# Performance work log

Measured on AMD Instinct MI355X. Metric: run time of the kernel, lower is better.

The kernel has to match this reference:

```python
import jax, jax.numpy as jnp
import numpy as np

N_NODES = 100000
N_EDGES = 1600000
IN_DIM = 48
HID = 16
N_CLASSES = 8


def _sage_conv(x, src, dst, W_l, W_r, b, n_nodes):
    # PyG SAGEConv (aggr='mean', root_weight=True):
    #   out_i = W_l @ mean_{j in N(i)} x_j + b + W_r @ x_i
    msg = x[src]                                              # [E, F]
    agg = jax.ops.segment_sum(msg, dst, num_segments=n_nodes)  # [N, F]
    deg = jax.ops.segment_sum(jnp.ones((src.shape[0],), x.dtype), dst,
                              num_segments=n_nodes)            # [N]
    agg = agg / jnp.maximum(deg, 1.0)[:, None]
    return agg @ W_l.T + b + x @ W_r.T


def setup_inputs() -> dict:
    key = jax.random.key(0)
    ks = jax.random.split(key, 10)
    def lin(k, out_d, in_d):
        s = 1.0 / np.sqrt(in_d)
        return jax.random.uniform(k, (out_d, in_d), jnp.float32, -s, s)
    x = jax.random.normal(ks[0], (N_NODES, IN_DIM), jnp.float32)
    edge_index = jax.random.randint(ks[1], (2, N_EDGES), 0, N_NODES, jnp.int64)
    return {
        "x": x,
        "edge_index": edge_index,
        "W1_l": lin(ks[2], HID, IN_DIM), "W1_r": lin(ks[3], HID, IN_DIM),
        "b1": jnp.zeros((HID,), jnp.float32),
        "W2_l": lin(ks[4], HID, HID), "W2_r": lin(ks[5], HID, HID),
        "b2": jnp.zeros((HID,), jnp.float32),
        "W3_l": lin(ks[6], N_CLASSES, HID), "W3_r": lin(ks[7], N_CLASSES, HID),
        "b3": jnp.zeros((N_CLASSES,), jnp.float32),
    }


def reference(x, edge_index, W1_l, W1_r, b1, W2_l, W2_r, b2, W3_l, W3_r, b3):
    src, dst = edge_index[0], edge_index[1]
    n = x.shape[0]
    # dropout is identity in deterministic/eval reference
    h = jax.nn.elu(_sage_conv(x, src, dst, W1_l, W1_r, b1, n))
    h = jax.nn.elu(_sage_conv(h, src, dst, W2_l, W2_r, b2, n))
    h = jax.nn.elu(_sage_conv(h, src, dst, W3_l, W3_r, b3, n))
    return jax.nn.log_softmax(h, axis=-1)
```

## Files before the change

### kernel.cpp

```cpp
#include <hip/hip_runtime.h>
#include <hip/hip_bf16.h>
#include <math.h>

#define N_IN   48
#define N_HID  16
#define N_CLS  8
#define CAP    48
#define NB_SHIFT 9
#define TILE   4096
#define WSTR   52

__device__ __forceinline__ float bf2f(unsigned short u) {
    union { unsigned int i; float f; } c;
    c.i = ((unsigned int)u) << 16;
    return c.f;
}
__device__ __forceinline__ unsigned short f2bf(float f) {
    unsigned int u = __float_as_uint(f);
    unsigned int r = u + 0x7FFFu + ((u >> 16) & 1u);
    return (unsigned short)(r >> 16);
}

__global__ __launch_bounds__(256) void proj48_kernel(
        const float* __restrict__ X,
        const float* __restrict__ Wl,
        const float* __restrict__ Wr,
        const float* __restrict__ b,
        unsigned short* __restrict__ P,
        float* __restrict__ S,
        int N) {
    __shared__ float sWl[N_HID * WSTR];
    __shared__ float sWr[N_HID * WSTR];
    __shared__ float sb[N_HID];
    int t = threadIdx.x;
    for (int idx = t; idx < N_HID * N_IN; idx += 256) {
        int r = idx / N_IN, k = idx - r * N_IN;
        sWl[r * WSTR + k] = Wl[idx];
        sWr[r * WSTR + k] = Wr[idx];
    }
    if (t < N_HID) sb[t] = b[t];
    __syncthreads();

    int node = blockIdx.x * 64 + (t >> 2);
    int q = t & 3;
    if (node >= N) return;

    const float4* xrow = reinterpret_cast<const float4*>(X + (size_t)node * N_IN);
    float accL[4], accR[4];
#pragma unroll
    for (int oo = 0; oo < 4; oo++) { accL[oo] = 0.0f; accR[oo] = sb[4 * q + oo]; }

#pragma unroll
    for (int c = 0; c < N_IN / 4; c++) {
        float4 xv = xrow[c];
#pragma unroll
        for (int oo = 0; oo < 4; oo++) {
            int row = 4 * q + oo;
            float4 wl = *reinterpret_cast<const float4*>(&sWl[row * WSTR + 4 * c]);
            float4 wr = *reinterpret_cast<const float4*>(&sWr[row * WSTR + 4 * c]);
            accL[oo] = fmaf(xv.x, wl.x, accL[oo]); accR[oo] = fmaf(xv.x, wr.x, accR[oo]);
            accL[oo] = fmaf(xv.y, wl.y, accL[oo]); accR[oo] = fmaf(xv.y, wr.y, accR[oo]);
            accL[oo] = fmaf(xv.z, wl.z, accL[oo]); accR[oo] = fmaf(xv.z, wr.z, accR[oo]);
            accL[oo] = fmaf(xv.w, wl.w, accL[oo]); accR[oo] = fmaf(xv.w, wr.w, accR[oo]);
        }
    }

    int gid = node * 4 + q;
    reinterpret_cast<ushort4*>(P)[gid] =
        make_ushort4(f2bf(accL[0]), f2bf(accL[1]), f2bf(accL[2]), f2bf(accL[3]));
    reinterpret_cast<float4*>(S)[gid] =
        make_float4(accR[0], accR[1], accR[2], accR[3]);
}

__global__ __launch_bounds__(256) void hist0_kernel(
        const int* __restrict__ dst, int* __restrict__ bucketCnt,
        int E, int nbuck) {
    __shared__ int lh[256];
    lh[threadIdx.x] = 0;
    __syncthreads();
    for (int e = blockIdx.x * blockDim.x + threadIdx.x; e < E;
         e += gridDim.x * blockDim.x)
        atomicAdd(&lh[dst[e] >> NB_SHIFT], 1);
    __syncthreads();
    int t = threadIdx.x;
    if (t < nbuck && lh[t]) atomicAdd(&bucketCnt[t], lh[t]);
}

__global__ __launch_bounds__(256) void scan_kernel(
        const int* __restrict__ bucketCnt, int* __restrict__ bucketBase,
        int* __restrict__ cursor, int nbuck, int E) {
    __shared__ int s[256];
    int t = threadIdx.x;
    int v = (t < nbuck) ? bucketCnt[t] : 0;
    s[t] = v;
    __syncthreads();
#pragma unroll
    for (int d = 1; d < 256; d <<= 1) {
        int a = (t >= d) ? s[t - d] : 0;
        __syncthreads();
        s[t] += a;
        __syncthreads();
    }
    if (t < nbuck) {
        int base = s[t] - v;
        bucketBase[t] = base;
        cursor[t] = base;
    }
    if (t == 0) bucketBase[nbuck] = E;
}

__global__ __launch_bounds__(256) void scatter_tiles_kernel(
        const int* __restrict__ src, const int* __restrict__ dst,
        int* __restrict__ cursor, int* __restrict__ ebuf, int E) {
    __shared__ int lh[256];
    __shared__ int gbase[256];
    __shared__ int rank[256];
    int t = threadIdx.x;
    lh[t] = 0;
    rank[t] = 0;
    __syncthreads();
    int base = blockIdx.x * TILE;
#pragma unroll
    for (int k = 0; k < TILE / 256; k++) {
        int e = base + t + k * 256;
        if (e < E) atomicAdd(&lh[dst[e] >> NB_SHIFT], 1);
    }
    __syncthreads();
    if (lh[t]) gbase[t] = atomicAdd(&cursor[t], lh[t]);
    __syncthreads();
#pragma unroll
    for (int k = 0; k < TILE / 256; k++) {
        int e = base + t + k * 256;
        if (e < E) {
            int d = dst[e];
            int b = d >> NB_SHIFT;
            int r = atomicAdd(&rank[b], 1);
            ebuf[gbase[b] + r] = ((d & 511) << 17) | src[e];
        }
    }
}

__global__ __launch_bounds__(256) void fine_fill_kernel(
        const int* __restrict__ bucketBase, const int* __restrict__ ebuf,
        int* __restrict__ cnt, int* __restrict__ adj, int N) {
    __shared__ int lc[512];
    int b = blockIdx.x;
    int nodeBeg = b << NB_SHIFT;
    for (int i = threadIdx.x; i < 512; i += 256) lc[i] = 0;
    __syncthreads();
    int beg = bucketBase[b], end = bucketBase[b + 1];
    for (int e = beg + threadIdx.x; e < end; e += 256) {
        int v = ebuf[e];
        int ld = ((unsigned int)v) >> 17;
        int s  = v & 0x1FFFF;
        int p = atomicAdd(&lc[ld], 1);
        if (p < CAP) adj[(size_t)(nodeBeg + ld) * CAP + p] = s;
    }
    __syncthreads();
    for (int i = threadIdx.x; nodeBeg + i < N && i < 512; i += 256)
        cnt[nodeBeg + i] = lc[i];
}

__global__ __launch_bounds__(256) void gather_proj16_kernel(
        const int* __restrict__ cnt, const int* __restrict__ adj,
        const unsigned short* __restrict__ Pin, const float* __restrict__ Sin,
        const float* __restrict__ Wl, const float* __restrict__ Wr,
        const float* __restrict__ bias,
        unsigned short* __restrict__ Pout, float* __restrict__ Sout, int N) {
    int gid = blockIdx.x * blockDim.x + threadIdx.x;
    if (gid >= N * 4) return;
    int i = gid >> 2;
    int q = gid & 3;
    int deg = cnt[i];
    if (deg > CAP) deg = CAP;
    const int* lst = adj + (size_t)i * CAP;
    float4 acc = make_float4(0.f, 0.f, 0.f, 0.f);
    const ushort4* P4 = reinterpret_cast<const ushort4*>(Pin);
    int e = 0;
    for (; e + 4 <= deg; e += 4) {
        int4 js = *reinterpret_cast<const int4*>(lst + e);
        ushort4 t0 = P4[(size_t)js.x * 4 + q];
        ushort4 t1 = P4[(size_t)js.y * 4 + q];
        ushort4 t2 = P4[(size_t)js.z * 4 + q];
        ushort4 t3 = P4[(size_t)js.w * 4 + q];
        acc.x += bf2f(t0.x) + bf2f(t1.x) + bf2f(t2.x) + bf2f(t3.x);
        acc.y += bf2f(t0.y) + bf2f(t1.y) + bf2f(t2.y) + bf2f(t3.y);
        acc.z += bf2f(t0.z) + bf2f(t1.z) + bf2f(t2.z) + bf2f(t3.z);
        acc.w += bf2f(t0.w) + bf2f(t1.w) + bf2f(t2.w) + bf2f(t3.w);
    }
    for (; e < deg; e++) {
        ushort4 t = P4[(size_t)lst[e] * 4 + q];
        acc.x += bf2f(t.x); acc.y += bf2f(t.y);
        acc.z += bf2f(t.z); acc.w += bf2f(t.w);
    }
    float inv = 1.0f / (float)max(deg, 1);
    float4 sv = reinterpret_cast<const float4*>(Sin)[gid];
    float4 h;
    h.x = acc.x * inv + sv.x; h.y = acc.y * inv + sv.y;
    h.z = acc.z * inv + sv.z; h.w = acc.w * inv + sv.w;
    h.x = h.x > 0.f ? h.x : expm1f(h.x);
    h.y = h.y > 0.f ? h.y : expm1f(h.y);
    h.z = h.z > 0.f ? h.z : expm1f(h.z);
    h.w = h.w > 0.f ? h.w : expm1f(h.w);

    int lane = threadIdx.x & 63;
    int lb = lane & ~3;
    float hv[16];
#pragma unroll
    for (int a = 0; a < 4; a++) {
        hv[4 * a + 0] = __shfl(h.x, lb + a, 64);
        hv[4 * a + 1] = __shfl(h.y, lb + a, 64);
        hv[4 * a + 2] = __shfl(h.z, lb + a, 64);
        hv[4 * a + 3] = __shfl(h.w, lb + a, 64);
    }

    const float4* Wl4 = reinterpret_cast<const float4*>(Wl);
    const float4* Wr4 = reinterpret_cast<const float4*>(Wr);
    float pl[4], sr[4];
#pragma unroll
    for (int oo = 0; oo < 4; oo++) {
        int o = 4 * q + oo;
        float aL = 0.0f, aR = bias[o];
#pragma unroll
        for (int c = 0; c < 4; c++) {
            float4 wl = Wl4[o * 4 + c];
            float4 wr = Wr4[o * 4 + c];
            aL = fmaf(hv[4 * c + 0], wl.x, aL); aR = fmaf(hv[4 * c + 0], wr.x, aR);
            aL = fmaf(hv[4 * c + 1], wl.y, aL); aR = fmaf(hv[4 * c + 1], wr.y, aR);
            aL = fmaf(hv[4 * c + 2], wl.z, aL); aR = fmaf(hv[4 * c + 2], wr.z, aR);
            aL = fmaf(hv[4 * c + 3], wl.w, aL); aR = fmaf(hv[4 * c + 3], wr.w, aR);
        }
        pl[oo] = aL; sr[oo] = aR;
    }
    reinterpret_cast<ushort4*>(Pout)[gid] =
        make_ushort4(f2bf(pl[0]), f2bf(pl[1]), f2bf(pl[2]), f2bf(pl[3]));
    reinterpret_cast<float4*>(Sout)[gid] = make_float4(sr[0], sr[1], sr[2], sr[3]);
}

__global__ __launch_bounds__(256) void gather_proj8_kernel(
        const int* __restrict__ cnt, const int* __restrict__ adj,
        const unsigned short* __restrict__ Pin, const float* __restrict__ Sin,
        const float* __restrict__ Wl, const float* __restrict__ Wr,
        const float* __restrict__ bias,
        unsigned short* __restrict__ Pout, float* __restrict__ Sout, int N) {
    int gid = blockIdx.x * blockDim.x + threadIdx.x;
    if (gid >= N * 4) return;
    int i = gid >> 2;
    int q = gid & 3;
    int deg = cnt[i];
    if (deg > CAP) deg = CAP;
    const int* lst = adj + (size_t)i * CAP;
    float4 acc = make_float4(0.f, 0.f, 0.f, 0.f);
    const ushort4* P4 = reinterpret_cast<const ushort4*>(Pin);
    int e = 0;
    for (; e + 4 <= deg; e += 4) {
        int4 js = *reinterpret_cast<const int4*>(lst + e);
        ushort4 t0 = P4[(size_t)js.x * 4 + q];
        ushort4 t1 = P4[(size_t)js.y * 4 + q];
        ushort4 t2 = P4[(size_t)js.z * 4 + q];
        ushort4 t3 = P4[(size_t)js.w * 4 + q];
        acc.x += bf2f(t0.x) + bf2f(t1.x) + bf2f(t2.x) + bf2f(t3.x);
        acc.y += bf2f(t0.y) + bf2f(t1.y) + bf2f(t2.y) + bf2f(t3.y);
        acc.z += bf2f(t0.z) + bf2f(t1.z) + bf2f(t2.z) + bf2f(t3.z);
        acc.w += bf2f(t0.w) + bf2f(t1.w) + bf2f(t2.w) + bf2f(t3.w);
    }
    for (; e < deg; e++) {
        ushort4 t = P4[(size_t)lst[e] * 4 + q];
        acc.x += bf2f(t.x); acc.y += bf2f(t.y);
        acc.z += bf2f(t.z); acc.w += bf2f(t.w);
    }
    float inv = 1.0f / (float)max(deg, 1);
    float4 sv = reinterpret_cast<const float4*>(Sin)[gid];
    float4 h;
    h.x = acc.x * inv + sv.x; h.y = acc.y * inv + sv.y;
    h.z = acc.z * inv + sv.z; h.w = acc.w * inv + sv.w;
    h.x = h.x > 0.f ? h.x : expm1f(h.x);
    h.y = h.y > 0.f ? h.y : expm1f(h.y);
    h.z = h.z > 0.f ? h.z : expm1f(h.z);
    h.w = h.w > 0.f ? h.w : expm1f(h.w);

    int lane = threadIdx.x & 63;
    int lb = lane & ~3;
    float hv[16];
#pragma unroll
    for (int a = 0; a < 4; a++) {
        hv[4 * a + 0] = __shfl(h.x, lb + a, 64);
        hv[4 * a + 1] = __shfl(h.y, lb + a, 64);
        hv[4 * a + 2] = __shfl(h.z, lb + a, 64);
        hv[4 * a + 3] = __shfl(h.w, lb + a, 64);
    }

    const float4* Wl4 = reinterpret_cast<const float4*>(Wl);
    const float4* Wr4 = reinterpret_cast<const float4*>(Wr);
    float pl[2], sr[2];
#pragma unroll
    for (int oo = 0; oo < 2; oo++) {
        int o = 2 * q + oo;
        float aL = 0.0f, aR = bias[o];
#pragma unroll
        for (int c = 0; c < 4; c++) {
            float4 wl = Wl4[o * 4 + c];
            float4 wr = Wr4[o * 4 + c];
            aL = fmaf(hv[4 * c + 0], wl.x, aL); aR = fmaf(hv[4 * c + 0], wr.x, aR);
            aL = fmaf(hv[4 * c + 1], wl.y, aL); aR = fmaf(hv[4 * c + 1], wr.y, aR);
            aL = fmaf(hv[4 * c + 2], wl.z, aL); aR = fmaf(hv[4 * c + 2], wr.z, aR);
            aL = fmaf(hv[4 * c + 3], wl.w, aL); aR = fmaf(hv[4 * c + 3], wr.w, aR);
        }
        pl[oo] = aL; sr[oo] = aR;
    }
    unsigned int packed = ((unsigned int)f2bf(pl[1]) << 16) | f2bf(pl[0]);
    reinterpret_cast<unsigned int*>(Pout)[gid] = packed;
    reinterpret_cast<float2*>(Sout)[gid] = make_float2(sr[0], sr[1]);
}

__global__ __launch_bounds__(256) void gather8_kernel(
        const int* __restrict__ cnt, const int* __restrict__ adj,
        const unsigned short* __restrict__ P, const float* __restrict__ S,
        float* __restrict__ out, int N) {
    int gid = blockIdx.x * blockDim.x + threadIdx.x;
    if (gid >= N * 2) return;
    int i = gid >> 1;
    int q = gid & 1;
    int deg = cnt[i];
    if (deg > CAP) deg = CAP;
    const int* lst = adj + (size_t)i * CAP;
    float4 acc = make_float4(0.f, 0.f, 0.f, 0.f);
    const ushort4* P4 = reinterpret_cast<const ushort4*>(P);
    int e = 0;
    for (; e + 4 <= deg; e += 4) {
        int4 js = *reinterpret_cast<const int4*>(lst + e);
        ushort4 t0 = P4[(size_t)js.x * 2 + q];
        ushort4 t1 = P4[(size_t)js.y * 2 + q];
        ushort4 t2 = P4[(size_t)js.z * 2 + q];
        ushort4 t3 = P4[(size_t)js.w * 2 + q];
        acc.x += bf2f(t0.x) + bf2f(t1.x) + bf2f(t2.x) + bf2f(t3.x);
        acc.y += bf2f(t0.y) + bf2f(t1.y) + bf2f(t2.y) + bf2f(t3.y);
        acc.z += bf2f(t0.z) + bf2f(t1.z) + bf2f(t2.z) + bf2f(t3.z);
        acc.w += bf2f(t0.w) + bf2f(t1.w) + bf2f(t2.w) + bf2f(t3.w);
    }
    for (; e < deg; e++) {
        ushort4 t = P4[(size_t)lst[e] * 2 + q];
        acc.x += bf2f(t.x); acc.y += bf2f(t.y);
        acc.z += bf2f(t.z); acc.w += bf2f(t.w);
    }
    float inv = 1.0f / (float)max(deg, 1);
    float4 sv = reinterpret_cast<const float4*>(S)[gid];
    float4 v;
    v.x = acc.x * inv + sv.x; v.y = acc.y * inv + sv.y;
    v.z = acc.z * inv + sv.z; v.w = acc.w * inv + sv.w;
    v.x = v.x > 0.f ? v.x : expm1f(v.x);
    v.y = v.y > 0.f ? v.y : expm1f(v.y);
    v.z = v.z > 0.f ? v.z : expm1f(v.z);
    v.w = v.w > 0.f ? v.w : expm1f(v.w);
    float m = fmaxf(fmaxf(v.x, v.y), fmaxf(v.z, v.w));
    m = fmaxf(m, __shfl_xor(m, 1));
    float sum = expf(v.x - m) + expf(v.y - m) + expf(v.z - m) + expf(v.w - m);
    sum += __shfl_xor(sum, 1);
    float lse = m + logf(sum);
    reinterpret_cast<float4*>(out)[gid] =
        make_float4(v.x - lse, v.y - lse, v.z - lse, v.w - lse);
}

extern "C" void kernel_launch(void* const* d_in, const int* in_sizes, int n_in,
                              void* d_out, int out_size, void* d_ws, size_t ws_size,
                              hipStream_t stream) {
    const float* x   = (const float*)d_in[0];
    const int*   ei  = (const int*)d_in[1];
    const float* W1l = (const float*)d_in[2];
    const float* W1r = (const float*)d_in[3];
    const float* b1  = (const float*)d_in[4];
    const float* W2l = (const float*)d_in[5];
    const float* W2r = (const float*)d_in[6];
    const float* b2  = (const float*)d_in[7];
    const float* W3l = (const float*)d_in[8];
    const float* W3r = (const float*)d_in[9];
    const float* b3  = (const float*)d_in[10];
    float* out = (float*)d_out;

    const int N = in_sizes[0] / N_IN;
    const int E = in_sizes[1] / 2;
    const int* src = ei;
    const int* dst = ei + E;
    const int nbuck = (N + 511) >> NB_SHIFT;

    int* bucketCnt  = (int*)d_ws;
    int* bucketBase = bucketCnt + 512;
    int* cursor     = bucketBase + 512;
    int* cnt        = cursor + 512;
    int  Npad       = (N + 3) & ~3;
    int* adj        = cnt + Npad;
    unsigned short* P1 = (unsigned short*)(adj + (size_t)N * CAP);
    unsigned short* P2 = P1 + (size_t)N * N_HID;
    float* S1 = (float*)(P2 + (size_t)N * N_HID);
    float* S3 = S1 + (size_t)N * N_HID;
    int* ebuf = (int*)P1;
    unsigned short* P3 = P1;

    hipMemsetAsync(bucketCnt, 0, 512 * sizeof(int), stream);

    const int B = 256;
    int n4Grid   = (N * 4 + B - 1) / B;
    int n2Grid   = (N * 2 + B - 1) / B;
    int p1Grid   = (N + 63) / 64;
    int tileGrid = (E + TILE - 1) / TILE;

    hist0_kernel<<<512, B, 0, stream>>>(dst, bucketCnt, E, nbuck);
    scan_kernel<<<1, 256, 0, stream>>>(bucketCnt, bucketBase, cursor, nbuck, E);
    scatter_tiles_kernel<<<tileGrid, B, 0, stream>>>(src, dst, cursor, ebuf, E);
    fine_fill_kernel<<<nbuck, B, 0, stream>>>(bucketBase, ebuf, cnt, adj, N);

    proj48_kernel<<<p1Grid, B, 0, stream>>>(x, W1l, W1r, b1, P1, S1, N);

    gather_proj16_kernel<<<n4Grid, B, 0, stream>>>(cnt, adj, P1, S1,
                                                   W2l, W2r, b2, P2, S1, N);

    gather_proj8_kernel<<<n4Grid, B, 0, stream>>>(cnt, adj, P2, S1,
                                                  W3l, W3r, b3, P3, S3, N);

    gather8_kernel<<<n2Grid, B, 0, stream>>>(cnt, adj, P3, S3, out, N);
}
```

Before: 258.0 us.

## Aggregate neighbors per destination bucket with LDS atomics instead of a per-node adjacency list

Drops the histogram, scan and fine-fill kernels and builds no per-node adjacency list. Edges are scattered into fixed-capacity slots per 512-node destination bucket. Each of the three layers then runs one 512-thread block per bucket that gathers source features and accumulates sums and degrees with shared-memory float atomics, then applies the projection or log-softmax. The root-term S buffers are also stored as bf16 instead of fp32, cutting memory traffic at some cost in precision. Risks: only about 196 blocks, which may underfill the GPU; shared-atomic contention; and silent edge loss if a bucket receives more than 9216 edges.

```diff
diff --git a/kernel.cpp b/kernel.cpp
--- a/kernel.cpp
+++ b/kernel.cpp
@@ -5,10 +5,13 @@
 #define N_IN   48
 #define N_HID  16
 #define N_CLS  8
-#define CAP    48
 #define NB_SHIFT 9
+#define BNODES 512
 #define TILE   4096
+#define CAPB   9216
 #define WSTR   52
+#define ASTR   17
+#define ASTR8  9
 
 __device__ __forceinline__ float bf2f(unsigned short u) {
     union { unsigned int i; float f; } c;
@@ -27,7 +30,7 @@
         const float* __restrict__ Wr,
         const float* __restrict__ b,
         unsigned short* __restrict__ P,
-        float* __restrict__ S,
+        unsigned short* __restrict__ S,
         int N) {
     __shared__ float sWl[N_HID * WSTR];
     __shared__ float sWr[N_HID * WSTR];
@@ -68,45 +71,8 @@
     int gid = node * 4 + q;
     reinterpret_cast<ushort4*>(P)[gid] =
         make_ushort4(f2bf(accL[0]), f2bf(accL[1]), f2bf(accL[2]), f2bf(accL[3]));
-    reinterpret_cast<float4*>(S)[gid] =
-        make_float4(accR[0], accR[1], accR[2], accR[3]);
-}
-
-__global__ __launch_bounds__(256) void hist0_kernel(
-        const int* __restrict__ dst, int* __restrict__ bucketCnt,
-        int E, int nbuck) {
-    __shared__ int lh[256];
-    lh[threadIdx.x] = 0;
-    __syncthreads();
-    for (int e = blockIdx.x * blockDim.x + threadIdx.x; e < E;
-         e += gridDim.x * blockDim.x)
-        atomicAdd(&lh[dst[e] >> NB_SHIFT], 1);
-    __syncthreads();
-    int t = threadIdx.x;
-    if (t < nbuck && lh[t]) atomicAdd(&bucketCnt[t], lh[t]);
-}
-
-__global__ __launch_bounds__(256) void scan_kernel(
-        const int* __restrict__ bucketCnt, int* __restrict__ bucketBase,
-        int* __restrict__ cursor, int nbuck, int E) {
-    __shared__ int s[256];
-    int t = threadIdx.x;
-    int v = (t < nbuck) ? bucketCnt[t] : 0;
-    s[t] = v;
-    __syncthreads();
-#pragma unroll
-    for (int d = 1; d < 256; d <<= 1) {
-        int a = (t >= d) ? s[t - d] : 0;
-        __syncthreads();
-        s[t] += a;
-        __syncthreads();
-    }
-    if (t < nbuck) {
-        int base = s[t] - v;
-        bucketBase[t] = base;
-        cursor[t] = base;
-    }
-    if (t == 0) bucketBase[nbuck] = E;
+    reinterpret_cast<ushort4*>(S)[gid] =
+        make_ushort4(f2bf(accR[0]), f2bf(accR[1]), f2bf(accR[2]), f2bf(accR[3]));
 }
 
 __global__ __launch_bounds__(256) void scatter_tiles_kernel(
@@ -120,10 +86,16 @@
     rank[t] = 0;
     __syncthreads();
     int base = blockIdx.x * TILE;
+    int dcache[TILE / 256];
 #pragma unroll
     for (int k = 0; k < TILE / 256; k++) {
         int e = base + t + k * 256;
-        if (e < E) atomicAdd(&lh[dst[e] >> NB_SHIFT], 1);
+        dcache[k] = -1;
+        if (e < E) {
+            int d = dst[e];
+            dcache[k] = d;
+            atomicAdd(&lh[d >> NB_SHIFT], 1);
+        }
     }
     __syncthreads();
     if (lh[t]) gbase[t] = atomicAdd(&cursor[t], lh[t]);
@@ -132,233 +104,275 @@
     for (int k = 0; k < TILE / 256; k++) {
         int e = base + t + k * 256;
         if (e < E) {
-            int d = dst[e];
+            int d = dcache[k];
             int b = d >> NB_SHIFT;
-            int r = atomicAdd(&rank[b], 1);
-            ebuf[gbase[b] + r] = ((d & 511) << 17) | src[e];
-        }
-    }
-}
-
-__global__ __launch_bounds__(256) void fine_fill_kernel(
-        const int* __restrict__ bucketBase, const int* __restrict__ ebuf,
-        int* __restrict__ cnt, int* __restrict__ adj, int N) {
-    __shared__ int lc[512];
-    int b = blockIdx.x;
-    int nodeBeg = b << NB_SHIFT;
-    for (int i = threadIdx.x; i < 512; i += 256) lc[i] = 0;
-    __syncthreads();
-    int beg = bucketBase[b], end = bucketBase[b + 1];
-    for (int e = beg + threadIdx.x; e < end; e += 256) {
-        int v = ebuf[e];
-        int ld = ((unsigned int)v) >> 17;
-        int s  = v & 0x1FFFF;
-        int p = atomicAdd(&lc[ld], 1);
-        if (p < CAP) adj[(size_t)(nodeBeg + ld) * CAP + p] = s;
-    }
-    __syncthreads();
-    for (int i = threadIdx.x; nodeBeg + i < N && i < 512; i += 256)
-        cnt[nodeBeg + i] = lc[i];
-}
-
-__global__ __launch_bounds__(256) void gather_proj16_kernel(
-        const int* __restrict__ cnt, const int* __restrict__ adj,
-        const unsigned short* __restrict__ Pin, const float* __restrict__ Sin,
+            int r = gbase[b] + atomicAdd(&rank[b], 1);
+            if (r < CAPB)
+                ebuf[b * CAPB + r] = ((d & 511) << 17) | src[e];
+        }
+    }
+}
+
+__global__ __launch_bounds__(512) void bucket_gp16_kernel(
+        const int* __restrict__ cursor, const int* __restrict__ ebuf,
+        const unsigned short* __restrict__ Pin, const unsigned short* __restrict__ Sin,
         const float* __restrict__ Wl, const float* __restrict__ Wr,
         const float* __restrict__ bias,
-        unsigned short* __restrict__ Pout, float* __restrict__ Sout, int N) {
-    int gid = blockIdx.x * blockDim.x + threadIdx.x;
-    if (gid >= N * 4) return;
-    int i = gid >> 2;
-    int q = gid & 3;
-    int deg = cnt[i];
-    if (deg > CAP) deg = CAP;
-    const int* lst = adj + (size_t)i * CAP;
-    float4 acc = make_float4(0.f, 0.f, 0.f, 0.f);
+        unsigned short* __restrict__ Pout, unsigned short* __restrict__ Sout, int N) {
+    __shared__ float agg[BNODES * ASTR];
+    __shared__ int   cnt[BNODES];
+    int b = blockIdx.x;
+    int t = threadIdx.x;
+    int nodeBeg = b << NB_SHIFT;
+    for (int i = t; i < BNODES * ASTR; i += 512) agg[i] = 0.0f;
+    if (t < BNODES) cnt[t] = 0;
+    __syncthreads();
+
+    int nb = cursor[b];
+    if (nb > CAPB) nb = CAPB;
+    int beg = b * CAPB, end = beg + nb;
+    int quad = t >> 2, q = t & 3;
     const ushort4* P4 = reinterpret_cast<const ushort4*>(Pin);
-    int e = 0;
-    for (; e + 4 <= deg; e += 4) {
-        int4 js = *reinterpret_cast<const int4*>(lst + e);
-        ushort4 t0 = P4[(size_t)js.x * 4 + q];
-        ushort4 t1 = P4[(size_t)js.y * 4 + q];
-        ushort4 t2 = P4[(size_t)js.z * 4 + q];
-        ushort4 t3 = P4[(size_t)js.w * 4 + q];
-        acc.x += bf2f(t0.x) + bf2f(t1.x) + bf2f(t2.x) + bf2f(t3.x);
-        acc.y += bf2f(t0.y) + bf2f(t1.y) + bf2f(t2.y) + bf2f(t3.y);
-        acc.z += bf2f(t0.z) + bf2f(t1.z) + bf2f(t2.z) + bf2f(t3.z);
-        acc.w += bf2f(t0.w) + bf2f(t1.w) + bf2f(t2.w) + bf2f(t3.w);
-    }
-    for (; e < deg; e++) {
-        ushort4 t = P4[(size_t)lst[e] * 4 + q];
-        acc.x += bf2f(t.x); acc.y += bf2f(t.y);
-        acc.z += bf2f(t.z); acc.w += bf2f(t.w);
-    }
-    float inv = 1.0f / (float)max(deg, 1);
-    float4 sv = reinterpret_cast<const float4*>(Sin)[gid];
-    float4 h;
-    h.x = acc.x * inv + sv.x; h.y = acc.y * inv + sv.y;
-    h.z = acc.z * inv + sv.z; h.w = acc.w * inv + sv.w;
-    h.x = h.x > 0.f ? h.x : expm1f(h.x);
-    h.y = h.y > 0.f ? h.y : expm1f(h.y);
-    h.z = h.z > 0.f ? h.z : expm1f(h.z);
-    h.w = h.w > 0.f ? h.w : expm1f(h.w);
-
-    int lane = threadIdx.x & 63;
-    int lb = lane & ~3;
-    float hv[16];
-#pragma unroll
-    for (int a = 0; a < 4; a++) {
-        hv[4 * a + 0] = __shfl(h.x, lb + a, 64);
-        hv[4 * a + 1] = __shfl(h.y, lb + a, 64);
-        hv[4 * a + 2] = __shfl(h.z, lb + a, 64);
-        hv[4 * a + 3] = __shfl(h.w, lb + a, 64);
-    }
+    int e = beg + quad;
+    for (; e + 128 < end; e += 256) {
+        int v0 = ebuf[e], v1 = ebuf[e + 128];
+        int ld0 = ((unsigned int)v0) >> 17, s0 = v0 & 0x1FFFF;
+        int ld1 = ((unsigned int)v1) >> 17, s1 = v1 & 0x1FFFF;
+        ushort4 p0 = P4[(size_t)s0 * 4 + q];
+        ushort4 p1 = P4[(size_t)s1 * 4 + q];
+        float* a0 = &agg[ld0 * ASTR + 4 * q];
+        float* a1 = &agg[ld1 * ASTR + 4 * q];
+        atomicAdd(a0 + 0, bf2f(p0.x)); atomicAdd(a0 + 1, bf2f(p0.y));
+        atomicAdd(a0 + 2, bf2f(p0.z)); atomicAdd(a0 + 3, bf2f(p0.w));
+        atomicAdd(a1 + 0, bf2f(p1.x)); atomicAdd(a1 + 1, bf2f(p1.y));
+        atomicAdd(a1 + 2, bf2f(p1.z)); atomicAdd(a1 + 3, bf2f(p1.w));
+        if (q == 0) { atomicAdd(&cnt[ld0], 1); atomicAdd(&cnt[ld1], 1); }
+    }
+    for (; e < end; e += 128) {
+        int v = ebuf[e];
+        int ld = ((unsigned int)v) >> 17, s = v & 0x1FFFF;
+        ushort4 p = P4[(size_t)s * 4 + q];
+        float* a = &agg[ld * ASTR + 4 * q];
+        atomicAdd(a + 0, bf2f(p.x)); atomicAdd(a + 1, bf2f(p.y));
+        atomicAdd(a + 2, bf2f(p.z)); atomicAdd(a + 3, bf2f(p.w));
+        if (q == 0) atomicAdd(&cnt[ld], 1);
+    }
+    __syncthreads();
 
     const float4* Wl4 = reinterpret_cast<const float4*>(Wl);
     const float4* Wr4 = reinterpret_cast<const float4*>(Wr);
-    float pl[4], sr[4];
-#pragma unroll
-    for (int oo = 0; oo < 4; oo++) {
-        int o = 4 * q + oo;
-        float aL = 0.0f, aR = bias[o];
-#pragma unroll
-        for (int c = 0; c < 4; c++) {
-            float4 wl = Wl4[o * 4 + c];
-            float4 wr = Wr4[o * 4 + c];
-            aL = fmaf(hv[4 * c + 0], wl.x, aL); aR = fmaf(hv[4 * c + 0], wr.x, aR);
-            aL = fmaf(hv[4 * c + 1], wl.y, aL); aR = fmaf(hv[4 * c + 1], wr.y, aR);
-            aL = fmaf(hv[4 * c + 2], wl.z, aL); aR = fmaf(hv[4 * c + 2], wr.z, aR);
-            aL = fmaf(hv[4 * c + 3], wl.w, aL); aR = fmaf(hv[4 * c + 3], wr.w, aR);
-        }
-        pl[oo] = aL; sr[oo] = aR;
-    }
-    reinterpret_cast<ushort4*>(Pout)[gid] =
-        make_ushort4(f2bf(pl[0]), f2bf(pl[1]), f2bf(pl[2]), f2bf(pl[3]));
-    reinterpret_cast<float4*>(Sout)[gid] = make_float4(sr[0], sr[1], sr[2], sr[3]);
-}
-
-__global__ __launch_bounds__(256) void gather_proj8_kernel(
-        const int* __restrict__ cnt, const int* __restrict__ adj,
-        const unsigned short* __restrict__ Pin, const float* __restrict__ Sin,
+#pragma unroll
+    for (int p = 0; p < 4; p++) {
+        int ln = p * 128 + (t >> 2);
+        int i = nodeBeg + ln;
+        if (i >= N) continue;
+        int gid = i * 4 + q;
+        int deg = cnt[ln];
+        float inv = 1.0f / (float)max(deg, 1);
+        ushort4 svu = reinterpret_cast<const ushort4*>(Sin)[gid];
+        float4 h;
+        h.x = agg[ln * ASTR + 4 * q + 0] * inv + bf2f(svu.x);
+        h.y = agg[ln * ASTR + 4 * q + 1] * inv + bf2f(svu.y);
+        h.z = agg[ln * ASTR + 4 * q + 2] * inv + bf2f(svu.z);
+        h.w = agg[ln * ASTR + 4 * q + 3] * inv + bf2f(svu.w);
+        h.x = h.x > 0.f ? h.x : expm1f(h.x);
+        h.y = h.y > 0.f ? h.y : expm1f(h.y);
+        h.z = h.z > 0.f ? h.z : expm1f(h.z);
+        h.w = h.w > 0.f ? h.w : expm1f(h.w);
+
+        int lane = t & 63;
+        int lb = lane & ~3;
+        float hv[16];
+#pragma unroll
+        for (int a = 0; a < 4; a++) {
+            hv[4 * a + 0] = __shfl(h.x, lb + a, 64);
+            hv[4 * a + 1] = __shfl(h.y, lb + a, 64);
+            hv[4 * a + 2] = __shfl(h.z, lb + a, 64);
+            hv[4 * a + 3] = __shfl(h.w, lb + a, 64);
+        }
+        float pl[4], sr[4];
+#pragma unroll
+        for (int oo = 0; oo < 4; oo++) {
+            int o = 4 * q + oo;
+            float aL = 0.0f, aR = bias[o];
+#pragma unroll
+            for (int c = 0; c < 4; c++) {
+                float4 wl = Wl4[o * 4 + c];
+                float4 wr = Wr4[o * 4 + c];
+                aL = fmaf(hv[4 * c + 0], wl.x, aL); aR = fmaf(hv[4 * c + 0], wr.x, aR);
+                aL = fmaf(hv[4 * c + 1], wl.y, aL); aR = fmaf(hv[4 * c + 1], wr.y, aR);
+                aL = fmaf(hv[4 * c + 2], wl.z, aL); aR = fmaf(hv[4 * c + 2], wr.z, aR);
+                aL = fmaf(hv[4 * c + 3], wl.w, aL); aR = fmaf(hv[4 * c + 3], wr.w, aR);
+            }
+            pl[oo] = aL; sr[oo] = aR;
+        }
+        reinterpret_cast<ushort4*>(Pout)[gid] =
+            make_ushort4(f2bf(pl[0]), f2bf(pl[1]), f2bf(pl[2]), f2bf(pl[3]));
+        reinterpret_cast<ushort4*>(Sout)[gid] =
+            make_ushort4(f2bf(sr[0]), f2bf(sr[1]), f2bf(sr[2]), f2bf(sr[3]));
+    }
+}
+
+__global__ __launch_bounds__(512) void bucket_gp8_kernel(
+        const int* __restrict__ cursor, const int* __restrict__ ebuf,
+        const unsigned short* __restrict__ Pin, const unsigned short* __restrict__ Sin,
         const float* __restrict__ Wl, const float* __restrict__ Wr,
         const float* __restrict__ bias,
-        unsigned short* __restrict__ Pout, float* __restrict__ Sout, int N) {
-    int gid = blockIdx.x * blockDim.x + threadIdx.x;
-    if (gid >= N * 4) return;
-    int i = gid >> 2;
-    int q = gid & 3;
-    int deg = cnt[i];
-    if (deg > CAP) deg = CAP;
-    const int* lst = adj + (size_t)i * CAP;
-    float4 acc = make_float4(0.f, 0.f, 0.f, 0.f);
+        unsigned int* __restrict__ Pout, unsigned int* __restrict__ Sout, int N) {
+    __shared__ float agg[BNODES * ASTR];
+    __shared__ int   cnt[BNODES];
+    int b = blockIdx.x;
+    int t = threadIdx.x;
+    int nodeBeg = b << NB_SHIFT;
+    for (int i = t; i < BNODES * ASTR; i += 512) agg[i] = 0.0f;
+    if (t < BNODES) cnt[t] = 0;
+    __syncthreads();
+
+    int nb = cursor[b];
+    if (nb > CAPB) nb = CAPB;
+    int beg = b * CAPB, end = beg + nb;
+    int quad = t >> 2, q = t & 3;
     const ushort4* P4 = reinterpret_cast<const ushort4*>(Pin);
-    int e = 0;
-    for (; e + 4 <= deg; e += 4) {
-        int4 js = *reinterpret_cast<const int4*>(lst + e);
-        ushort4 t0 = P4[(size_t)js.x * 4 + q];
-        ushort4 t1 = P4[(size_t)js.y * 4 + q];
-        ushort4 t2 = P4[(size_t)js.z * 4 + q];
-        ushort4 t3 = P4[(size_t)js.w * 4 + q];
-        acc.x += bf2f(t0.x) + bf2f(t1.x) + bf2f(t2.x) + bf2f(t3.x);
-        acc.y += bf2f(t0.y) + bf2f(t1.y) + bf2f(t2.y) + bf2f(t3.y);
-        acc.z += bf2f(t0.z) + bf2f(t1.z) + bf2f(t2.z) + bf2f(t3.z);
-        acc.w += bf2f(t0.w) + bf2f(t1.w) + bf2f(t2.w) + bf2f(t3.w);
-    }
-    for (; e < deg; e++) {
-        ushort4 t = P4[(size_t)lst[e] * 4 + q];
-        acc.x += bf2f(t.x); acc.y += bf2f(t.y);
-        acc.z += bf2f(t.z); acc.w += bf2f(t.w);
-    }
-    float inv = 1.0f / (float)max(deg, 1);
-    float4 sv = reinterpret_cast<const float4*>(Sin)[gid];
-    float4 h;
-    h.x = acc.x * inv + sv.x; h.y = acc.y * inv + sv.y;
-    h.z = acc.z * inv + sv.z; h.w = acc.w * inv + sv.w;
-    h.x = h.x > 0.f ? h.x : expm1f(h.x);
-    h.y = h.y > 0.f ? h.y : expm1f(h.y);
-    h.z = h.z > 0.f ? h.z : expm1f(h.z);
-    h.w = h.w > 0.f ? h.w : expm1f(h.w);
-
-    int lane = threadIdx.x & 63;
-    int lb = lane & ~3;
-    float hv[16];
-#pragma unroll
-    for (int a = 0; a < 4; a++) {
-        hv[4 * a + 0] = __shfl(h.x, lb + a, 64);
-        hv[4 * a + 1] = __shfl(h.y, lb + a, 64);
-        hv[4 * a + 2] = __shfl(h.z, lb + a, 64);
-        hv[4 * a + 3] = __shfl(h.w, lb + a, 64);
-    }
+    int e = beg + quad;
+    for (; e + 128 < end; e += 256) {
+        int v0 = ebuf[e], v1 = ebuf[e + 128];
+        int ld0 = ((unsigned int)v0) >> 17, s0 = v0 & 0x1FFFF;
+        int ld1 = ((unsigned int)v1) >> 17, s1 = v1 & 0x1FFFF;
+        ushort4 p0 = P4[(size_t)s0 * 4 + q];
+        ushort4 p1 = P4[(size_t)s1 * 4 + q];
+        float* a0 = &agg[ld0 * ASTR + 4 * q];
+        float* a1 = &agg[ld1 * ASTR + 4 * q];
+        atomicAdd(a0 + 0, bf2f(p0.x)); atomicAdd(a0 + 1, bf2f(p0.y));
+        atomicAdd(a0 + 2, bf2f(p0.z)); atomicAdd(a0 + 3, bf2f(p0.w));
+        atomicAdd(a1 + 0, bf2f(p1.x)); atomicAdd(a1 + 1, bf2f(p1.y));
+        atomicAdd(a1 + 2, bf2f(p1.z)); atomicAdd(a1 + 3, bf2f(p1.w));
+        if (q == 0) { atomicAdd(&cnt[ld0], 1); atomicAdd(&cnt[ld1], 1); }
+    }
+    for (; e < end; e += 128) {
+        int v = ebuf[e];
+        int ld = ((unsigned int)v) >> 17, s = v & 0x1FFFF;
+        ushort4 p = P4[(size_t)s * 4 + q];
+        float* a = &agg[ld * ASTR + 4 * q];
+        atomicAdd(a + 0, bf2f(p.x)); atomicAdd(a + 1, bf2f(p.y));
+        atomicAdd(a + 2, bf2f(p.z)); atomicAdd(a + 3, bf2f(p.w));
+        if (q == 0) atomicAdd(&cnt[ld], 1);
+    }
+    __syncthreads();
 
     const float4* Wl4 = reinterpret_cast<const float4*>(Wl);
     const float4* Wr4 = reinterpret_cast<const float4*>(Wr);
-    float pl[2], sr[2];
-#pragma unroll
-    for (int oo = 0; oo < 2; oo++) {
-        int o = 2 * q + oo;
-        float aL = 0.0f, aR = bias[o];
-#pragma unroll
-        for (int c = 0; c < 4; c++) {
-            float4 wl = Wl4[o * 4 + c];
-            float4 wr = Wr4[o * 4 + c];
-            aL = fmaf(hv[4 * c + 0], wl.x, aL); aR = fmaf(hv[4 * c + 0], wr.x, aR);
-            aL = fmaf(hv[4 * c + 1], wl.y, aL); aR = fmaf(hv[4 * c + 1], wr.y, aR);
-            aL = fmaf(hv[4 * c + 2], wl.z, aL); aR = fmaf(hv[4 * c + 2], wr.z, aR);
-            aL = fmaf(hv[4 * c + 3], wl.w, aL); aR = fmaf(hv[4 * c + 3], wr.w, aR);
-        }
-        pl[oo] = aL; sr[oo] = aR;
-    }
-    unsigned int packed = ((unsigned int)f2bf(pl[1]) << 16) | f2bf(pl[0]);
-    reinterpret_cast<unsigned int*>(Pout)[gid] = packed;
-    reinterpret_cast<float2*>(Sout)[gid] = make_float2(sr[0], sr[1]);
-}
-
-__global__ __launch_bounds__(256) void gather8_kernel(
-        const int* __restrict__ cnt, const int* __restrict__ adj,
-        const unsigned short* __restrict__ P, const float* __restrict__ S,
+#pragma unroll
+    for (int p = 0; p < 4; p++) {
+        int ln = p * 128 + (t >> 2);
+        int i = nodeBeg + ln;
+        if (i >= N) continue;
+        int gid = i * 4 + q;
+        int deg = cnt[ln];
+        float inv = 1.0f / (float)max(deg, 1);
+        ushort4 svu = reinterpret_cast<const ushort4*>(Sin)[gid];
+        float4 h;
+        h.x = agg[ln * ASTR + 4 * q + 0] * inv + bf2f(svu.x);
+        h.y = agg[ln * ASTR + 4 * q + 1] * inv + bf2f(svu.y);
+        h.z = agg[ln * ASTR + 4 * q + 2] * inv + bf2f(svu.z);
+        h.w = agg[ln * ASTR + 4 * q + 3] * inv + bf2f(svu.w);
+        h.x = h.x > 0.f ? h.x : expm1f(h.x);
+        h.y = h.y > 0.f ? h.y : expm1f(h.y);
+        h.z = h.z > 0.f ? h.z : expm1f(h.z);
+        h.w = h.w > 0.f ? h.w : expm1f(h.w);
+
+        int lane = t & 63;
+        int lb = lane & ~3;
+        float hv[16];
+#pragma unroll
+        for (int a = 0; a < 4; a++) {
+            hv[4 * a + 0] = __shfl(h.x, lb + a, 64);
+            hv[4 * a + 1] = __shfl(h.y, lb + a, 64);
+            hv[4 * a + 2] = __shfl(h.z, lb + a, 64);
+            hv[4 * a + 3] = __shfl(h.w, lb + a, 64);
+        }
+        float pl[2], sr[2];
+#pragma unroll
+        for (int oo = 0; oo < 2; oo++) {
+            int o = 2 * q + oo;
+            float aL = 0.0f, aR = bias[o];
+#pragma unroll
+            for (int c = 0; c < 4; c++) {
+                float4 wl = Wl4[o * 4 + c];
+                float4 wr = Wr4[o * 4 + c];
+                aL = fmaf(hv[4 * c + 0], wl.x, aL); aR = fmaf(hv[4 * c + 0], wr.x, aR);
+                aL = fmaf(hv[4 * c + 1], wl.y, aL); aR = fmaf(hv[4 * c + 1], wr.y, aR);
+                aL = fmaf(hv[4 * c + 2], wl.z, aL); aR = fmaf(hv[4 * c + 2], wr.z, aR);
+                aL = fmaf(hv[4 * c + 3], wl.w, aL); aR = fmaf(hv[4 * c + 3], wr.w, aR);
+            }
+            pl[oo] = aL; sr[oo] = aR;
+        }
+        Pout[gid] = ((unsigned int)f2bf(pl[1]) << 16) | f2bf(pl[0]);
+        Sout[gid] = ((unsigned int)f2bf(sr[1]) << 16) | f2bf(sr[0]);
+    }
+}
+
+__global__ __launch_bounds__(512) void bucket_out_kernel(
+        const int* __restrict__ cursor, const int* __restrict__ ebuf,
+        const unsigned int* __restrict__ Pin, const unsigned int* __restrict__ Sin,
         float* __restrict__ out, int N) {
-    int gid = blockIdx.x * blockDim.x + threadIdx.x;
-    if (gid >= N * 2) return;
-    int i = gid >> 1;
-    int q = gid & 1;
-    int deg = cnt[i];
-    if (deg > CAP) deg = CAP;
-    const int* lst = adj + (size_t)i * CAP;
-    float4 acc = make_float4(0.f, 0.f, 0.f, 0.f);
-    const ushort4* P4 = reinterpret_cast<const ushort4*>(P);
-    int e = 0;
-    for (; e + 4 <= deg; e += 4) {
-        int4 js = *reinterpret_cast<const int4*>(lst + e);
-        ushort4 t0 = P4[(size_t)js.x * 2 + q];
-        ushort4 t1 = P4[(size_t)js.y * 2 + q];
-        ushort4 t2 = P4[(size_t)js.z * 2 + q];
-        ushort4 t3 = P4[(size_t)js.w * 2 + q];
-        acc.x += bf2f(t0.x) + bf2f(t1.x) + bf2f(t2.x) + bf2f(t3.x);
-        acc.y += bf2f(t0.y) + bf2f(t1.y) + bf2f(t2.y) + bf2f(t3.y);
-        acc.z += bf2f(t0.z) + bf2f(t1.z) + bf2f(t2.z) + bf2f(t3.z);
-        acc.w += bf2f(t0.w) + bf2f(t1.w) + bf2f(t2.w) + bf2f(t3.w);
-    }
-    for (; e < deg; e++) {
-        ushort4 t = P4[(size_t)lst[e] * 2 + q];
-        acc.x += bf2f(t.x); acc.y += bf2f(t.y);
-        acc.z += bf2f(t.z); acc.w += bf2f(t.w);
-    }
-    float inv = 1.0f / (float)max(deg, 1);
-    float4 sv = reinterpret_cast<const float4*>(S)[gid];
-    float4 v;
-    v.x = acc.x * inv + sv.x; v.y = acc.y * inv + sv.y;
-    v.z = acc.z * inv + sv.z; v.w = acc.w * inv + sv.w;
-    v.x = v.x > 0.f ? v.x : expm1f(v.x);
-    v.y = v.y > 0.f ? v.y : expm1f(v.y);
-    v.z = v.z > 0.f ? v.z : expm1f(v.z);
-    v.w = v.w > 0.f ? v.w : expm1f(v.w);
-    float m = fmaxf(fmaxf(v.x, v.y), fmaxf(v.z, v.w));
-    m = fmaxf(m, __shfl_xor(m, 1));
-    float sum = expf(v.x - m) + expf(v.y - m) + expf(v.z - m) + expf(v.w - m);
-    sum += __shfl_xor(sum, 1);
-    float lse = m + logf(sum);
-    reinterpret_cast<float4*>(out)[gid] =
-        make_float4(v.x - lse, v.y - lse, v.z - lse, v.w - lse);
+    __shared__ float agg[BNODES * ASTR8];
+    __shared__ int   cnt[BNODES];
+    int b = blockIdx.x;
+    int t = threadIdx.x;
+    int nodeBeg = b << NB_SHIFT;
+    for (int i = t; i < BNODES * ASTR8; i += 512) agg[i] = 0.0f;
+    if (t < BNODES) cnt[t] = 0;
+    __syncthreads();
+
+    int nb = cursor[b];
+    if (nb > CAPB) nb = CAPB;
+    int beg = b * CAPB, end = beg + nb;
+    int quad = t >> 2, q = t & 3;
+    int e = beg + quad;
+    for (; e + 128 < end; e += 256) {
+        int v0 = ebuf[e], v1 = ebuf[e + 128];
+        int ld0 = ((unsigned int)v0) >> 17, s0 = v0 & 0x1FFFF;
+        int ld1 = ((unsigned int)v1) >> 17, s1 = v1 & 0x1FFFF;
+        unsigned int u0 = Pin[(size_t)s0 * 4 + q];
+        unsigned int u1 = Pin[(size_t)s1 * 4 + q];
+        atomicAdd(&agg[ld0 * ASTR8 + 2 * q + 0], bf2f((unsigned short)(u0 & 0xFFFF)));
+        atomicAdd(&agg[ld0 * ASTR8 + 2 * q + 1], bf2f((unsigned short)(u0 >> 16)));
+        atomicAdd(&agg[ld1 * ASTR8 + 2 * q + 0], bf2f((unsigned short)(u1 & 0xFFFF)));
+        atomicAdd(&agg[ld1 * ASTR8 + 2 * q + 1], bf2f((unsigned short)(u1 >> 16)));
+        if (q == 0) { atomicAdd(&cnt[ld0], 1); atomicAdd(&cnt[ld1], 1); }
+    }
+    for (; e < end; e += 128) {
+        int v = ebuf[e];
+        int ld = ((unsigned int)v) >> 17, s = v & 0x1FFFF;
+        unsigned int u = Pin[(size_t)s * 4 + q];
+        atomicAdd(&agg[ld * ASTR8 + 2 * q + 0], bf2f((unsigned short)(u & 0xFFFF)));
+        atomicAdd(&agg[ld * ASTR8 + 2 * q + 1], bf2f((unsigned short)(u >> 16)));
+        if (q == 0) atomicAdd(&cnt[ld], 1);
+    }
+    __syncthreads();
+
+#pragma unroll
+    for (int p = 0; p < 4; p++) {
+        int ln = p * 128 + (t >> 2);
+        int i = nodeBeg + ln;
+        if (i >= N) continue;
+        int gid = i * 4 + q;
+        int deg = cnt[ln];
+        float inv = 1.0f / (float)max(deg, 1);
+        unsigned int su = Sin[gid];
+        float v0 = agg[ln * ASTR8 + 2 * q + 0] * inv + bf2f((unsigned short)(su & 0xFFFF));
+        float v1 = agg[ln * ASTR8 + 2 * q + 1] * inv + bf2f((unsigned short)(su >> 16));
+        v0 = v0 > 0.f ? v0 : expm1f(v0);
+        v1 = v1 > 0.f ? v1 : expm1f(v1);
+        float m = fmaxf(v0, v1);
+        m = fmaxf(m, __shfl_xor(m, 1));
+        m = fmaxf(m, __shfl_xor(m, 2));
+        float sum = expf(v0 - m) + expf(v1 - m);
+        sum += __shfl_xor(sum, 1);
+        sum += __shfl_xor(sum, 2);
+        float lse = m + logf(sum);
+        reinterpret_cast<float2*>(out)[gid] = make_float2(v0 - lse, v1 - lse);
+    }
 }
 
 extern "C" void kernel_launch(void* const* d_in, const int* in_sizes, int n_in,
@@ -381,41 +395,35 @@
     const int E = in_sizes[1] / 2;
     const int* src = ei;
     const int* dst = ei + E;
-    const int nbuck = (N + 511) >> NB_SHIFT;
-
-    int* bucketCnt  = (int*)d_ws;
-    int* bucketBase = bucketCnt + 512;
-    int* cursor     = bucketBase + 512;
-    int* cnt        = cursor + 512;
-    int  Npad       = (N + 3) & ~3;
-    int* adj        = cnt + Npad;
-    unsigned short* P1 = (unsigned short*)(adj + (size_t)N * CAP);
+    const int nbuck = (N + BNODES - 1) >> NB_SHIFT;
+
+    int* cursor = (int*)d_ws;
+    int* ebuf   = cursor + 256;
+    unsigned short* P1 = (unsigned short*)(ebuf + (size_t)nbuck * CAPB);
     unsigned short* P2 = P1 + (size_t)N * N_HID;
-    float* S1 = (float*)(P2 + (size_t)N * N_HID);
-    float* S3 = S1 + (size_t)N * N_HID;
-    int* ebuf = (int*)P1;
+    unsigned short* S1 = P2 + (size_t)N * N_HID;
+    unsigned short* S3 = S1 + (size_t)N * N_HID;
     unsigned short* P3 = P1;
 
-    hipMemsetAsync(bucketCnt, 0, 512 * sizeof(int), stream);
+    hipMemsetAsync(cursor, 0, 256 * sizeof(int), stream);
 
     const int B = 256;
-    int n4Grid   = (N * 4 + B - 1) / B;
-    int n2Grid   = (N * 2 + B - 1) / B;
     int p1Grid   = (N + 63) / 64;
     int tileGrid = (E + TILE - 1) / TILE;
 
-    hist0_kernel<<<512, B, 0, stream>>>(dst, bucketCnt, E, nbuck);
-    scan_kernel<<<1, 256, 0, stream>>>(bucketCnt, bucketBase, cursor, nbuck, E);
     scatter_tiles_kernel<<<tileGrid, B, 0, stream>>>(src, dst, cursor, ebuf, E);
-    fine_fill_kernel<<<nbuck, B, 0, stream>>>(bucketBase, ebuf, cnt, adj, N);
 
     proj48_kernel<<<p1Grid, B, 0, stream>>>(x, W1l, W1r, b1, P1, S1, N);
 
-    gather_proj16_kernel<<<n4Grid, B, 0, stream>>>(cnt, adj, P1, S1,
-                                                   W2l, W2r, b2, P2, S1, N);
-
-    gather_proj8_kernel<<<n4Grid, B, 0, stream>>>(cnt, adj, P2, S1,
-                                                  W3l, W3r, b3, P3, S3, N);
-
-    gather8_kernel<<<n2Grid, B, 0, stream>>>(cnt, adj, P3, S3, out, N);
-}
+    bucket_gp16_kernel<<<nbuck, 512, 0, stream>>>(cursor, ebuf, P1, S1,
+                                                  W2l, W2r, b2, P2, S1, N);
+
+    bucket_gp8_kernel<<<nbuck, 512, 0, stream>>>(cursor, ebuf, P2, S1,
+                                                 W3l, W3r, b3,
+                                                 (unsigned int*)P3,
+                                                 (unsigned int*)S3, N);
+
+    bucket_out_kernel<<<nbuck, 512, 0, stream>>>(cursor, ebuf,
+                                                 (const unsigned int*)P3,
+                                                 (const unsigned int*)S3, out, N);
+}
```

After: 608.4 us. 2.36x slower.
